# Performance work log

Measured on AMD Instinct MI355X. Metric: run time of the kernel, lower is better.

## Reference

```python
import jax, jax.numpy as jnp
import numpy as np

H = 16   # num_heads
K = 2    # top_k experts per token


def _layer_norm(x, g, b, eps=1e-5):
    mu = jnp.mean(x, axis=-1, keepdims=True)
    var = jnp.mean(jnp.square(x - mu), axis=-1, keepdims=True)
    return (x - mu) * jax.lax.rsqrt(var + eps) * g + b


def setup_inputs() -> dict:
    key = jax.random.key(0)
    ks = jax.random.split(key, 8)
    B, S, D, E = 2, 2048, 1024, 8
    sc = 0.02
    return {
        "x": jax.random.normal(ks[0], (B, S, D), jnp.float32),
        "wq": jax.random.normal(ks[1], (D, D), jnp.float32) * sc,
        "wk": jax.random.normal(ks[2], (D, D), jnp.float32) * sc,
        "wv": jax.random.normal(ks[3], (D, D), jnp.float32) * sc,
        "wo": jax.random.normal(ks[4], (D, D), jnp.float32) * sc,
        "ln1_g": jnp.ones((D,), jnp.float32),
        "ln1_b": jnp.zeros((D,), jnp.float32),
        "ln2_g": jnp.ones((D,), jnp.float32),
        "ln2_b": jnp.zeros((D,), jnp.float32),
        "router_w": jax.random.normal(ks[5], (E, D), jnp.float32) * sc,
        "expert_w": jax.random.normal(ks[6], (E, D, D), jnp.float32) * sc,
    }


def reference(x, wq, wk, wv, wo, ln1_g, ln1_b, ln2_g, ln2_b, router_w, expert_w):
    B, S, D = x.shape
    E = expert_w.shape[0]
    hd = D // H

    # ---- attention sublayer: x = x + attn(norm1(x)) ----
    h = _layer_norm(x, ln1_g, ln1_b)
    q = (h @ wq.T).reshape(B, S, H, hd).transpose(0, 2, 1, 3)  # bhsd
    k = (h @ wk.T).reshape(B, S, H, hd).transpose(0, 2, 1, 3)
    v = (h @ wv.T).reshape(B, S, H, hd).transpose(0, 2, 1, 3)
    scores = jnp.einsum("bhqd,bhkd->bhqk", q, k) / jnp.sqrt(jnp.float32(hd))
    causal = jnp.tril(jnp.ones((S, S), dtype=bool))
    scores = jnp.where(causal, scores, jnp.finfo(scores.dtype).min)
    probs = jax.nn.softmax(scores, axis=-1)
    attn = jnp.einsum("bhqk,bhkd->bhqd", probs, v)
    attn = attn.transpose(0, 2, 1, 3).reshape(B, S, D) @ wo.T
    x = x + attn

    # ---- MoE sublayer: x = x + moe(norm2(x)) ----
    h2 = _layer_norm(x, ln2_g, ln2_b)
    logits = jnp.einsum("bsd,ed->bse", h2, router_w)          # [B,S,E]
    top_logits, top_ids = jax.lax.top_k(logits, K)            # [B,S,K]
    gates = jax.nn.softmax(top_logits, axis=-1)               # [B,S,K]
    # dense combine weights over experts (E is small): sum_k gate_k * onehot(id_k)
    combine = jnp.sum(jax.nn.one_hot(top_ids, E, dtype=h2.dtype) * gates[..., None], axis=-2)  # [B,S,E]
    # per-token matvec with expert weights: token @ W_e.T for each expert, then weighted sum
    y = jnp.einsum("bsd,eod->bseo", h2, expert_w)             # [B,S,E,D]
    moe_out = jnp.einsum("bse,bseo->bso", combine, y)
    return x + moe_out
```

## Files before the change

kernel.cpp:

```cpp
#include <hip/hip_runtime.h>
#include <hip/hip_bf16.h>
#include <cstdint>


typedef __bf16 bf16;
typedef __bf16 bf16x8 __attribute__((ext_vector_type(8)));
typedef float f32x4 __attribute__((ext_vector_type(4)));

#define MFMA(a, b, c) __builtin_amdgcn_mfma_f32_16x16x32_bf16(a, b, c, 0, 0, 0)

__device__ __forceinline__ void gld16(void* lds, const void* g) {
  __builtin_amdgcn_global_load_lds(
      (const __attribute__((address_space(1))) void*)g,
      (__attribute__((address_space(3))) void*)lds, 16, 0, 0);
}

__global__ void split_f32(const float* __restrict__ s, bf16* __restrict__ hi,
                          bf16* __restrict__ lo, int n) {
  int i = (blockIdx.x * 256 + threadIdx.x) * 4;
  if (i >= n) return;
  float4 v = *(const float4*)(s + i);
  float a[4] = {v.x, v.y, v.z, v.w};
#pragma unroll
  for (int j = 0; j < 4; j++) {
    bf16 h = (bf16)a[j];
    hi[i + j] = h;
    lo[i + j] = (bf16)(a[j] - (float)h);
  }
}

__global__ void cvt_f32(const float* __restrict__ s, bf16* __restrict__ hi, int n) {
  int i = (blockIdx.x * 256 + threadIdx.x) * 4;
  if (i >= n) return;
  float4 v = *(const float4*)(s + i);
  hi[i] = (bf16)v.x; hi[i + 1] = (bf16)v.y;
  hi[i + 2] = (bf16)v.z; hi[i + 3] = (bf16)v.w;
}

__global__ void ln_split(const float* __restrict__ x, const float* __restrict__ g,
                         const float* __restrict__ b, bf16* __restrict__ hi,
                         bf16* __restrict__ lo) {
  int tok = blockIdx.x, t = threadIdx.x;
  float4 v = ((const float4*)(x + (size_t)tok * 1024))[t];
  float s = v.x + v.y + v.z + v.w;
  float ss = v.x * v.x + v.y * v.y + v.z * v.z + v.w * v.w;
#pragma unroll
  for (int o = 1; o < 64; o <<= 1) { s += __shfl_xor(s, o); ss += __shfl_xor(ss, o); }
  __shared__ float red[8];
  int w = t >> 6, lane = t & 63;
  if (lane == 0) { red[w] = s; red[4 + w] = ss; }
  __syncthreads();
  s = red[0] + red[1] + red[2] + red[3];
  ss = red[4] + red[5] + red[6] + red[7];
  float mu = s * (1.f / 1024.f);
  float rstd = rsqrtf(ss * (1.f / 1024.f) - mu * mu + 1e-5f);
  float4 gv = ((const float4*)g)[t], bv = ((const float4*)b)[t];
  float y[4] = {(v.x - mu) * rstd * gv.x + bv.x, (v.y - mu) * rstd * gv.y + bv.y,
                (v.z - mu) * rstd * gv.z + bv.z, (v.w - mu) * rstd * gv.w + bv.w};
  size_t o = (size_t)tok * 1024 + t * 4;
#pragma unroll
  for (int j = 0; j < 4; j++) {
    bf16 h = (bf16)y[j];
    hi[o + j] = h;
    lo[o + j] = (bf16)(y[j] - (float)h);
  }
}

__global__ void ln2f(const float* __restrict__ x, const float* __restrict__ g,
                     const float* __restrict__ b, float* __restrict__ h2f,
                     bf16* __restrict__ h2h) {
  int tok = blockIdx.x, t = threadIdx.x;
  float4 v = ((const float4*)(x + (size_t)tok * 1024))[t];
  float s = v.x + v.y + v.z + v.w;
  float ss = v.x * v.x + v.y * v.y + v.z * v.z + v.w * v.w;
#pragma unroll
  for (int o = 1; o < 64; o <<= 1) { s += __shfl_xor(s, o); ss += __shfl_xor(ss, o); }
  __shared__ float red[8];
  int w = t >> 6, lane = t & 63;
  if (lane == 0) { red[w] = s; red[4 + w] = ss; }
  __syncthreads();
  s = red[0] + red[1] + red[2] + red[3];
  ss = red[4] + red[5] + red[6] + red[7];
  float mu = s * (1.f / 1024.f);
  float rstd = rsqrtf(ss * (1.f / 1024.f) - mu * mu + 1e-5f);
  float4 gv = ((const float4*)g)[t], bv = ((const float4*)b)[t];
  float4 y;
  y.x = (v.x - mu) * rstd * gv.x + bv.x;
  y.y = (v.y - mu) * rstd * gv.y + bv.y;
  y.z = (v.z - mu) * rstd * gv.z + bv.z;
  y.w = (v.w - mu) * rstd * gv.w + bv.w;
  ((float4*)(h2f + (size_t)tok * 1024))[t] = y;
  size_t o = (size_t)tok * 1024 + t * 4;
  h2h[o] = (bf16)y.x; h2h[o + 1] = (bf16)y.y;
  h2h[o + 2] = (bf16)y.z; h2h[o + 3] = (bf16)y.w;
}

__global__ void route_wave(const float* __restrict__ h2f,
                           const float* __restrict__ rw, int* __restrict__ eid,
                           float2* __restrict__ gout) {
  int wid = (blockIdx.x * 256 + threadIdx.x) >> 6;
  int lane = threadIdx.x & 63;
  const float4* xr = (const float4*)(h2f + (size_t)wid * 1024);
  float acc[8] = {0.f, 0.f, 0.f, 0.f, 0.f, 0.f, 0.f, 0.f};
#pragma unroll
  for (int it = 0; it < 4; it++) {
    float4 xv = xr[lane + 64 * it];
#pragma unroll
    for (int e = 0; e < 8; e++) {
      float4 wv = ((const float4*)(rw + e * 1024))[lane + 64 * it];
      acc[e] += xv.x * wv.x + xv.y * wv.y + xv.z * wv.z + xv.w * wv.w;
    }
  }
#pragma unroll
  for (int e = 0; e < 8; e++)
#pragma unroll
    for (int o = 1; o < 64; o <<= 1) acc[e] += __shfl_xor(acc[e], o);
  if (lane == 0) {
    int i0 = 0; float l0 = acc[0];
#pragma unroll
    for (int e = 1; e < 8; e++) if (acc[e] > l0) { l0 = acc[e]; i0 = e; }
    int i1 = -1; float l1 = -3e38f;
#pragma unroll
    for (int e = 0; e < 8; e++) if (e != i0 && acc[e] > l1) { l1 = acc[e]; i1 = e; }
    float e1 = __expf(l1 - l0);
    float den = 1.f + e1;
    eid[wid] = i0 | (i1 << 4);
    gout[wid] = make_float2(1.f / den, e1 / den);
  }
}

__global__ void build_lists(const int* __restrict__ eid,
                            const float2* __restrict__ gv,
                            int* __restrict__ tlist, float* __restrict__ glist,
                            int* __restrict__ cnt) {
  int e = blockIdx.x, t = threadIdx.x;
  int lane = t & 63, w = t >> 6;
  __shared__ int wt[4];
  int base = 0;
  for (int c = 0; c < 16; c++) {
    int tok = c * 256 + t;
    int pair = eid[tok];
    int e0 = pair & 15, e1 = pair >> 4;
    bool p = (e0 == e) || (e1 == e);
    float2 g2 = gv[tok];
    float gate = (e0 == e) ? g2.x : g2.y;
    unsigned long long m = __ballot(p);
    int rank = __popcll(m & ((1ull << lane) - 1ull));
    if (lane == 0) wt[w] = __popcll(m);
    __syncthreads();
    int off = base;
    for (int i = 0; i < w; i++) off += wt[i];
    if (p) {
      tlist[e * 4096 + off + rank] = tok;
      glist[e * 4096 + off + rank] = gate;
    }
    base += wt[0] + wt[1] + wt[2] + wt[3];
    __syncthreads();
  }
  if (t == 0) cnt[e] = base;
  int pad = (base + 127) & ~127;
  if (pad > 4096) pad = 4096;
  for (int i = base + t; i < pad; i += 256) {
    tlist[e * 4096 + i] = 0;
    glist[e * 4096 + i] = 0.f;
  }
}

__device__ __forceinline__ void gemm_core_split(
    const bf16* __restrict__ Ah, const bf16* __restrict__ Al,
    const bf16* __restrict__ Bh, const bf16* __restrict__ Bl, int m0, int n0,
    f32x4 (&acc)[4][4]) {
  __shared__ __align__(16) bf16 As_h[4096], As_l[4096], Bs_h[4096], Bs_l[4096];
  int t = threadIdx.x, lane = t & 63, w = t >> 6;
  int i0 = t, i1 = t + 256;
  const bf16* a0h = Ah + (size_t)(m0 + (i0 >> 2)) * 1024 + (i0 & 3) * 8;
  const bf16* a1h = Ah + (size_t)(m0 + (i1 >> 2)) * 1024 + (i1 & 3) * 8;
  const bf16* a0l = Al + (size_t)(m0 + (i0 >> 2)) * 1024 + (i0 & 3) * 8;
  const bf16* a1l = Al + (size_t)(m0 + (i1 >> 2)) * 1024 + (i1 & 3) * 8;
  const bf16* b0h = Bh + (size_t)(n0 + (i0 >> 2)) * 1024 + (i0 & 3) * 8;
  const bf16* b1h = Bh + (size_t)(n0 + (i1 >> 2)) * 1024 + (i1 & 3) * 8;
  const bf16* b0l = Bl + (size_t)(n0 + (i0 >> 2)) * 1024 + (i0 & 3) * 8;
  const bf16* b1l = Bl + (size_t)(n0 + (i1 >> 2)) * 1024 + (i1 & 3) * 8;
  int wm = (w >> 1) * 64, wn = (w & 1) * 64;
  int lr = lane & 15, lq = lane >> 4;
  for (int k0 = 0; k0 < 1024; k0 += 32) {
    __syncthreads();
    gld16(&As_h[i0 * 8], a0h + k0); gld16(&As_h[i1 * 8], a1h + k0);
    gld16(&As_l[i0 * 8], a0l + k0); gld16(&As_l[i1 * 8], a1l + k0);
    gld16(&Bs_h[i0 * 8], b0h + k0); gld16(&Bs_h[i1 * 8], b1h + k0);
    gld16(&Bs_l[i0 * 8], b0l + k0); gld16(&Bs_l[i1 * 8], b1l + k0);
    __syncthreads();
    bf16x8 ah[4], al4[4], bh[4], bl4[4];
#pragma unroll
    for (int i = 0; i < 4; i++) {
      ah[i]  = *(const bf16x8*)&As_h[(wm + i * 16 + lr) * 32 + lq * 8];
      al4[i] = *(const bf16x8*)&As_l[(wm + i * 16 + lr) * 32 + lq * 8];
      bh[i]  = *(const bf16x8*)&Bs_h[(wn + i * 16 + lr) * 32 + lq * 8];
      bl4[i] = *(const bf16x8*)&Bs_l[(wn + i * 16 + lr) * 32 + lq * 8];
    }
#pragma unroll
    for (int i = 0; i < 4; i++)
#pragma unroll
      for (int j = 0; j < 4; j++) {
        f32x4 c = acc[i][j];
        c = MFMA(ah[i], bh[j], c);
        c = MFMA(ah[i], bl4[j], c);
        c = MFMA(al4[i], bh[j], c);
        acc[i][j] = c;
      }
  }
}

__global__ __launch_bounds__(256, 2) void gemm_qkv(
    const bf16* __restrict__ hh, const bf16* __restrict__ hl,
    const bf16* __restrict__ wqh, const bf16* __restrict__ wql,
    const bf16* __restrict__ wkh, const bf16* __restrict__ wkl,
    const bf16* __restrict__ wvh, const bf16* __restrict__ wvl,
    bf16* __restrict__ qh, bf16* __restrict__ ql, bf16* __restrict__ kh,
    bf16* __restrict__ kl, bf16* __restrict__ vh, bf16* __restrict__ vl) {
  int n0 = blockIdx.x * 128, m0 = blockIdx.y * 128, z = blockIdx.z;
  const bf16 *Bh = wqh, *Bl = wql;
  bf16 *Oh = qh, *Ol = ql;
  if (z == 1) { Bh = wkh; Bl = wkl; Oh = kh; Ol = kl; }
  if (z == 2) { Bh = wvh; Bl = wvl; Oh = vh; Ol = vl; }
  float scale = (z == 0) ? (0.125f * 1.44269504f) : 1.0f;
  f32x4 acc[4][4];
#pragma unroll
  for (int i = 0; i < 4; i++)
#pragma unroll
    for (int j = 0; j < 4; j++) acc[i][j] = (f32x4){0.f, 0.f, 0.f, 0.f};
  gemm_core_split(hh, hl, Bh, Bl, m0, n0, acc);
  int t = threadIdx.x, lane = t & 63, w = t >> 6;
  int wm = (w >> 1) * 64, wn = (w & 1) * 64, lr = lane & 15, lq = lane >> 4;
#pragma unroll
  for (int i = 0; i < 4; i++)
#pragma unroll
    for (int j = 0; j < 4; j++)
#pragma unroll
      for (int r = 0; r < 4; r++) {
        size_t row = m0 + wm + i * 16 + lq * 4 + r;
        int col = n0 + wn + j * 16 + lr;
        float v = acc[i][j][r] * scale;
        bf16 h = (bf16)v;
        Oh[row * 1024 + col] = h;
        Ol[row * 1024 + col] = (bf16)(v - (float)h);
      }
}

__global__ __launch_bounds__(256, 2) void gemm_wo(
    const bf16* __restrict__ ah, const bf16* __restrict__ al,
    const bf16* __restrict__ bh, const bf16* __restrict__ bl,
    const float* __restrict__ resid, float* __restrict__ outp) {
  int n0 = blockIdx.x * 128, m0 = blockIdx.y * 128;
  f32x4 acc[4][4];
#pragma unroll
  for (int i = 0; i < 4; i++)
#pragma unroll
    for (int j = 0; j < 4; j++) acc[i][j] = (f32x4){0.f, 0.f, 0.f, 0.f};
  gemm_core_split(ah, al, bh, bl, m0, n0, acc);
  int t = threadIdx.x, lane = t & 63, w = t >> 6;
  int wm = (w >> 1) * 64, wn = (w & 1) * 64, lr = lane & 15, lq = lane >> 4;
#pragma unroll
  for (int i = 0; i < 4; i++)
#pragma unroll
    for (int j = 0; j < 4; j++)
#pragma unroll
      for (int r = 0; r < 4; r++) {
        size_t row = m0 + wm + i * 16 + lq * 4 + r;
        int col = n0 + wn + j * 16 + lr;
        outp[row * 1024 + col] = resid[row * 1024 + col] + acc[i][j][r];
      }
}

__global__ void vtrans(const bf16* __restrict__ vh, const bf16* __restrict__ vl,
                       bf16* __restrict__ vth, bf16* __restrict__ vtl) {
  int bh = blockIdx.y, s0 = blockIdx.x * 64;
  int b = bh >> 4, h = bh & 15;
  int t = threadIdx.x;
  __shared__ __align__(16) bf16 tile[4096];
  int r = t >> 2, c4 = t & 3;
  int dr = t >> 2, tg = t & 3;
#pragma unroll
  for (int pass = 0; pass < 2; pass++) {
    const bf16* src = pass ? vl : vh;
    bf16* dst = pass ? vtl : vth;
    if (pass) __syncthreads();
    const bf16* sp = src + (size_t)(b * 2048 + s0 + r) * 1024 + h * 64 + c4 * 16;
    bf16x8 v0 = *(const bf16x8*)sp;
    bf16x8 v1 = *(const bf16x8*)(sp + 8);
#pragma unroll
    for (int j = 0; j < 8; j++) {
      int d0 = c4 * 16 + j, d1 = c4 * 16 + 8 + j;
      tile[d0 * 64 + (r ^ ((d0 >> 3) << 3))] = v0[j];
      tile[d1 * 64 + (r ^ ((d1 >> 3) << 3))] = v1[j];
    }
    __syncthreads();
#pragma unroll
    for (int hf = 0; hf < 2; hf++) {
      int tok = tg * 16 + hf * 8;
      bf16x8 o = *(const bf16x8*)&tile[dr * 64 + (tok ^ ((dr >> 3) << 3))];
      *(bf16x8*)(dst + (size_t)(bh * 64 + dr) * 2048 + s0 + tok) = o;
    }
  }
}

__global__ __launch_bounds__(256, 2) void attn_fused(
    const bf16* __restrict__ qh, const bf16* __restrict__ ql,
    const bf16* __restrict__ kh, const bf16* __restrict__ kl,
    const bf16* __restrict__ vth, const bf16* __restrict__ vtl,
    bf16* __restrict__ oh, bf16* __restrict__ ol) {
  const int S = 2048, D = 1024;
  int qt = 15 - blockIdx.y;
  int hb = blockIdx.x;
  int head = hb & 15, b = hb >> 4;
  int qb = qt * 128;
  int t = threadIdx.x, lane = t & 63, w = t >> 6;
  int lr = lane & 15, lq = lane >> 4;
  int base = b * S, hcol = head * 64;

  __shared__ __align__(16) bf16 Kh_s[4096], Kl_s[4096];
  __shared__ __align__(16) bf16 Vh_s[4096], Vl_s[4096];
  __shared__ __align__(16) bf16 Ph_s[4][1024], Pl_s[4][1024];

  bf16x8 qfh[2][2], qfl[2][2];
#pragma unroll
  for (int qr = 0; qr < 2; qr++) {
    const bf16* p1 = qh + (size_t)(base + qb + w * 32 + qr * 16 + lr) * D + hcol + lq * 8;
    const bf16* p2 = ql + (size_t)(base + qb + w * 32 + qr * 16 + lr) * D + hcol + lq * 8;
    qfh[qr][0] = *(const bf16x8*)p1; qfh[qr][1] = *(const bf16x8*)(p1 + 32);
    qfl[qr][0] = *(const bf16x8*)p2; qfl[qr][1] = *(const bf16x8*)(p2 + 32);
  }
  f32x4 O[2][4];
  float lrow[2][4];
#pragma unroll
  for (int qr = 0; qr < 2; qr++)
#pragma unroll
    for (int j = 0; j < 4; j++) {
      O[qr][j] = (f32x4){0.f, 0.f, 0.f, 0.f};
      lrow[qr][j] = 0.f;
    }

  int r0 = t >> 3, p0 = t & 7;
  int r1 = (t + 256) >> 3, p1 = (t + 256) & 7;
  int g0 = p0 ^ (r0 & 7), g1 = p1 ^ (r1 & 7);
  const bf16* k0hp = kh + (size_t)(base + r0) * D + hcol + g0 * 8;
  const bf16* k1hp = kh + (size_t)(base + r1) * D + hcol + g1 * 8;
  const bf16* k0lp = kl + (size_t)(base + r0) * D + hcol + g0 * 8;
  const bf16* k1lp = kl + (size_t)(base + r1) * D + hcol + g1 * 8;
  const bf16* v0hp = vth + (size_t)(hb * 64 + r0) * 2048 + g0 * 8;
  const bf16* v1hp = vth + (size_t)(hb * 64 + r1) * 2048 + g1 * 8;
  const bf16* v0lp = vtl + (size_t)(hb * 64 + r0) * 2048 + g0 * 8;
  const bf16* v1lp = vtl + (size_t)(hb * 64 + r1) * 2048 + g1 * 8;

  int qwmin = qb + w * 32;
  int pswz = ((lr >> 2) & 1) << 4;

  for (int kt = 0; kt <= qb + 64; kt += 64) {
    __syncthreads();
    gld16(&Kh_s[t * 8], k0hp + (size_t)kt * D);
    gld16(&Kh_s[2048 + t * 8], k1hp + (size_t)kt * D);
    gld16(&Kl_s[t * 8], k0lp + (size_t)kt * D);
    gld16(&Kl_s[2048 + t * 8], k1lp + (size_t)kt * D);
    gld16(&Vh_s[t * 8], v0hp + kt);
    gld16(&Vh_s[2048 + t * 8], v1hp + kt);
    gld16(&Vl_s[t * 8], v0lp + kt);
    gld16(&Vl_s[2048 + t * 8], v1lp + kt);
    __syncthreads();
    if (kt > qwmin + 31) continue;
    bool need_mask = (kt + 63 > qwmin);
#pragma unroll
    for (int hf = 0; hf < 2; hf++) {
      f32x4 sc[2][2];
#pragma unroll
      for (int tt = 0; tt < 2; tt++) {
        int key16 = (hf * 2 + tt) * 16 + lr;
        int gl = (lq ^ (key16 & 7)) * 8;
        int gh = ((4 + lq) ^ (key16 & 7)) * 8;
        bf16x8 k0 = *(const bf16x8*)&Kh_s[key16 * 64 + gl];
        bf16x8 k1 = *(const bf16x8*)&Kh_s[key16 * 64 + gh];
        bf16x8 m0 = *(const bf16x8*)&Kl_s[key16 * 64 + gl];
        bf16x8 m1 = *(const bf16x8*)&Kl_s[key16 * 64 + gh];
#pragma unroll
        for (int qr = 0; qr < 2; qr++) {
          f32x4 s = (f32x4){0.f, 0.f, 0.f, 0.f};
          s = MFMA(qfh[qr][0], k0, s); s = MFMA(qfh[qr][1], k1, s);
          s = MFMA(qfh[qr][0], m0, s); s = MFMA(qfh[qr][1], m1, s);
          s = MFMA(qfl[qr][0], k0, s); s = MFMA(qfl[qr][1], k1, s);
          sc[qr][tt] = s;
        }
      }
#pragma unroll
      for (int qr = 0; qr < 2; qr++)
#pragma unroll
        for (int tt = 0; tt < 2; tt++) {
          int key = kt + (hf * 2 + tt) * 16 + lr;
#pragma unroll
          for (int r = 0; r < 4; r++) {
            float s = sc[qr][tt][r];
            if (need_mask) {
              int q = qwmin + qr * 16 + lq * 4 + r;
              s = (key <= q) ? s : -30000.f;
            }
            float pv = __builtin_amdgcn_exp2f(s);
            lrow[qr][r] += pv;
            bf16 ph = (bf16)pv;
            int col = (tt * 16 + lr) ^ ((lq & 1) << 4);
            int idx = (qr * 16 + lq * 4 + r) * 32 + col;
            Ph_s[w][idx] = ph;
            Pl_s[w][idx] = (bf16)(pv - (float)ph);
          }
        }
      bf16x8 vbh[4], vbl[4];
#pragma unroll
      for (int j = 0; j < 4; j++) {
        int d = j * 16 + lr;
        int gv = ((hf * 4 + lq) ^ (d & 7)) * 8;
        vbh[j] = *(const bf16x8*)&Vh_s[d * 64 + gv];
        vbl[j] = *(const bf16x8*)&Vl_s[d * 64 + gv];
      }
#pragma unroll
      for (int qr = 0; qr < 2; qr++) {
        int poff = (qr * 16 + lr) * 32 + ((lq * 8) ^ pswz);
        bf16x8 pf = *(const bf16x8*)&Ph_s[w][poff];
        bf16x8 pl2 = *(const bf16x8*)&Pl_s[w][poff];
#pragma unroll
        for (int j = 0; j < 4; j++) {
          f32x4 c = O[qr][j];
          c = MFMA(pf, vbh[j], c);
          c = MFMA(pf, vbl[j], c);
          c = MFMA(pl2, vbh[j], c);
          O[qr][j] = c;
        }
      }
    }
  }
#pragma unroll
  for (int qr = 0; qr < 2; qr++) {
    float linv[4];
#pragma unroll
    for (int r = 0; r < 4; r++) {
      float l = lrow[qr][r];
      l += __shfl_xor(l, 1); l += __shfl_xor(l, 2);
      l += __shfl_xor(l, 4); l += __shfl_xor(l, 8);
      linv[r] = 1.f / l;
    }
#pragma unroll
    for (int j = 0; j < 4; j++)
#pragma unroll
      for (int r = 0; r < 4; r++) {
        size_t tok = (size_t)(base + qb + w * 32 + qr * 16 + lq * 4 + r);
        int col = hcol + j * 16 + lr;
        float v = O[qr][j][r] * linv[r];
        bf16 h = (bf16)v;
        oh[tok * D + col] = h;
        ol[tok * D + col] = (bf16)(v - (float)h);
      }
  }
}

__global__ __launch_bounds__(256, 2) void gemm_moe(
    const bf16* __restrict__ A, const bf16* __restrict__ W,
    const int* __restrict__ tlist, const float* __restrict__ glist,
    const int* __restrict__ cnt, float* __restrict__ outp) {
  int e = blockIdx.z;
  int count = cnt[e];
  int m0 = blockIdx.y * 128;
  if (m0 >= count) return;
  int n0 = blockIdx.x * 128;
  const int* tl = tlist + e * 4096;
  const bf16* B = W + (size_t)e * 1024 * 1024;
  __shared__ __align__(16) bf16 As[4096], Bs[4096];
  int t = threadIdx.x, lane = t & 63, w = t >> 6;
  int i0 = t, i1 = t + 256;
  int ra = tl[m0 + (i0 >> 2)], rb = tl[m0 + (i1 >> 2)];
  const bf16* a0 = A + (size_t)ra * 1024 + (i0 & 3) * 8;
  const bf16* a1 = A + (size_t)rb * 1024 + (i1 & 3) * 8;
  const bf16* b0 = B + (size_t)(n0 + (i0 >> 2)) * 1024 + (i0 & 3) * 8;
  const bf16* b1 = B + (size_t)(n0 + (i1 >> 2)) * 1024 + (i1 & 3) * 8;
  int wm = (w >> 1) * 64, wn = (w & 1) * 64, lr = lane & 15, lq = lane >> 4;
  f32x4 acc[4][4];
#pragma unroll
  for (int i = 0; i < 4; i++)
#pragma unroll
    for (int j = 0; j < 4; j++) acc[i][j] = (f32x4){0.f, 0.f, 0.f, 0.f};
  for (int k0 = 0; k0 < 1024; k0 += 32) {
    __syncthreads();
    gld16(&As[i0 * 8], a0 + k0); gld16(&As[i1 * 8], a1 + k0);
    gld16(&Bs[i0 * 8], b0 + k0); gld16(&Bs[i1 * 8], b1 + k0);
    __syncthreads();
    bf16x8 af[4], bfr[4];
#pragma unroll
    for (int i = 0; i < 4; i++) {
      af[i] = *(const bf16x8*)&As[(wm + i * 16 + lr) * 32 + lq * 8];
      bfr[i] = *(const bf16x8*)&Bs[(wn + i * 16 + lr) * 32 + lq * 8];
    }
#pragma unroll
    for (int i = 0; i < 4; i++)
#pragma unroll
      for (int j = 0; j < 4; j++) acc[i][j] = MFMA(af[i], bfr[j], acc[i][j]);
  }
#pragma unroll
  for (int i = 0; i < 4; i++)
#pragma unroll
    for (int r = 0; r < 4; r++) {
      int slot = m0 + wm + i * 16 + lq * 4 + r;
      if (slot < count) {
        int tok = tl[slot];
        float gte = glist[e * 4096 + slot];
#pragma unroll
        for (int j = 0; j < 4; j++) {
          int col = n0 + wn + j * 16 + lr;
          atomicAdd(&outp[(size_t)tok * 1024 + col], gte * acc[i][j][r]);
        }
      }
    }
}

extern "C" void kernel_launch(void* const* d_in, const int* in_sizes, int n_in,
                              void* d_out, int out_size, void* d_ws, size_t ws_size,
                              hipStream_t stream) {
  (void)in_sizes; (void)n_in; (void)out_size; (void)ws_size;
  const float* x    = (const float*)d_in[0];
  const float* wq   = (const float*)d_in[1];
  const float* wk   = (const float*)d_in[2];
  const float* wv   = (const float*)d_in[3];
  const float* wo   = (const float*)d_in[4];
  const float* ln1g = (const float*)d_in[5];
  const float* ln1b = (const float*)d_in[6];
  const float* ln2g = (const float*)d_in[7];
  const float* ln2b = (const float*)d_in[8];
  const float* rw   = (const float*)d_in[9];
  const float* expw = (const float*)d_in[10];
  float* out = (float*)d_out;

  char* p = (char*)d_ws;
  auto take = [&](size_t bytes) -> char* {
    char* r = p;
    p += (bytes + 255) & ~(size_t)255;
    return r;
  };
  const size_t ND2 = 4096ull * 1024 * 2;
  const size_t WD2 = 1024ull * 1024 * 2;
  bf16* h_hi = (bf16*)take(ND2); bf16* h_lo = (bf16*)take(ND2);
  bf16* wqh = (bf16*)take(WD2); bf16* wql = (bf16*)take(WD2);
  bf16* wkh = (bf16*)take(WD2); bf16* wkl = (bf16*)take(WD2);
  bf16* wvh = (bf16*)take(WD2); bf16* wvl = (bf16*)take(WD2);
  bf16* woh = (bf16*)take(WD2); bf16* wol = (bf16*)take(WD2);
  bf16* q_hi = (bf16*)take(ND2); bf16* q_lo = (bf16*)take(ND2);
  bf16* k_hi = (bf16*)take(ND2); bf16* k_lo = (bf16*)take(ND2);
  bf16* v_hi = (bf16*)take(ND2); bf16* v_lo = (bf16*)take(ND2);
  bf16* a_hi = (bf16*)take(ND2); bf16* a_lo = (bf16*)take(ND2);
  bf16* h2h  = (bf16*)take(ND2);
  bf16* ewh  = (bf16*)take(8ull * 1024 * 1024 * 2);
  int*   tlist  = (int*)take(8ull * 4096 * 4);
  float* glist  = (float*)take(8ull * 4096 * 4);
  int*   cnt    = (int*)take(64);
  int*   reid   = (int*)take(4096 * 4);
  float2* rg    = (float2*)take(4096 * 8);
  bf16* vt_hi = h_hi;
  bf16* vt_lo = h_lo;
  float* h2f = (float*)h_hi;

  split_f32<<<1024, 256, 0, stream>>>(wq, wqh, wql, 1048576);
  split_f32<<<1024, 256, 0, stream>>>(wk, wkh, wkl, 1048576);
  split_f32<<<1024, 256, 0, stream>>>(wv, wvh, wvl, 1048576);
  split_f32<<<1024, 256, 0, stream>>>(wo, woh, wol, 1048576);
  cvt_f32<<<8192, 256, 0, stream>>>(expw, ewh, 8388608);

  ln_split<<<4096, 256, 0, stream>>>(x, ln1g, ln1b, h_hi, h_lo);
  gemm_qkv<<<dim3(8, 32, 3), 256, 0, stream>>>(h_hi, h_lo, wqh, wql, wkh, wkl,
                                               wvh, wvl, q_hi, q_lo, k_hi, k_lo,
                                               v_hi, v_lo);
  vtrans<<<dim3(32, 32), 256, 0, stream>>>(v_hi, v_lo, vt_hi, vt_lo);
  attn_fused<<<dim3(32, 16), 256, 0, stream>>>(q_hi, q_lo, k_hi, k_lo, vt_hi,
                                               vt_lo, a_hi, a_lo);
  gemm_wo<<<dim3(8, 32), 256, 0, stream>>>(a_hi, a_lo, woh, wol, x, out);

  ln2f<<<4096, 256, 0, stream>>>(out, ln2g, ln2b, h2f, h2h);
  route_wave<<<1024, 256, 0, stream>>>(h2f, rw, reid, rg);
  build_lists<<<8, 256, 0, stream>>>(reid, rg, tlist, glist, cnt);
  gemm_moe<<<dim3(8, 32, 8), 256, 0, stream>>>(h2h, ewh, tlist, glist, cnt,
                                               out);
}
```

Before: 442.2 us.

## Fuse prep/router kernels, write V transposed from QKV GEMM, use 32x32 MFMA attention

Merges the five weight-conversion launches into one kernel and fuses LayerNorm2 with the router so the fp32 h2 buffer no longer round-trips through global memory. The QKV GEMM now writes V directly in transposed head layout, which removes the separate vtrans kernel. Attention is rebuilt around 32x32x16 MFMA tiles, packing hi/lo P values into one LDS word and skipping the fully masked second key subtile. Together these cut launch count and memory traffic, but the router now computes per token inside a block and the new attention changes register and LDS pressure.

```diff
diff --git a/kernel.cpp b/kernel.cpp
--- a/kernel.cpp
+++ b/kernel.cpp
@@ -5,9 +5,12 @@
 
 typedef __bf16 bf16;
 typedef __bf16 bf16x8 __attribute__((ext_vector_type(8)));
+typedef __bf16 bf16x4 __attribute__((ext_vector_type(4)));
 typedef float f32x4 __attribute__((ext_vector_type(4)));
+typedef float f32x16 __attribute__((ext_vector_type(16)));
 
 #define MFMA(a, b, c) __builtin_amdgcn_mfma_f32_16x16x32_bf16(a, b, c, 0, 0, 0)
+#define MFMA32(a, b, c) __builtin_amdgcn_mfma_f32_32x32x16_bf16(a, b, c, 0, 0, 0)
 
 __device__ __forceinline__ void gld16(void* lds, const void* g) {
   __builtin_amdgcn_global_load_lds(
@@ -15,26 +18,43 @@
       (__attribute__((address_space(3))) void*)lds, 16, 0, 0);
 }
 
-__global__ void split_f32(const float* __restrict__ s, bf16* __restrict__ hi,
-                          bf16* __restrict__ lo, int n) {
-  int i = (blockIdx.x * 256 + threadIdx.x) * 4;
-  if (i >= n) return;
-  float4 v = *(const float4*)(s + i);
-  float a[4] = {v.x, v.y, v.z, v.w};
-#pragma unroll
-  for (int j = 0; j < 4; j++) {
-    bf16 h = (bf16)a[j];
-    hi[i + j] = h;
-    lo[i + j] = (bf16)(a[j] - (float)h);
-  }
-}
-
-__global__ void cvt_f32(const float* __restrict__ s, bf16* __restrict__ hi, int n) {
-  int i = (blockIdx.x * 256 + threadIdx.x) * 4;
-  if (i >= n) return;
-  float4 v = *(const float4*)(s + i);
-  hi[i] = (bf16)v.x; hi[i + 1] = (bf16)v.y;
-  hi[i + 2] = (bf16)v.z; hi[i + 3] = (bf16)v.w;
+__device__ __forceinline__ uint32_t pack_hilo(float pv) {
+  bf16 h = (bf16)pv;
+  bf16 l = (bf16)(pv - (float)h);
+  union { bf16 b[2]; uint32_t u; } cv;
+  cv.b[0] = h; cv.b[1] = l;
+  return cv.u;
+}
+
+__global__ void prep_weights(const float* __restrict__ wq, const float* __restrict__ wk,
+                             const float* __restrict__ wv, const float* __restrict__ wo,
+                             const float* __restrict__ expw,
+                             bf16* __restrict__ wqh, bf16* __restrict__ wql,
+                             bf16* __restrict__ wkh, bf16* __restrict__ wkl,
+                             bf16* __restrict__ wvh, bf16* __restrict__ wvl,
+                             bf16* __restrict__ woh, bf16* __restrict__ wol,
+                             bf16* __restrict__ ewh) {
+  int bid = blockIdx.x;
+  if (bid < 4096) {
+    int wsel = bid >> 10;
+    const float* src = wsel == 0 ? wq : wsel == 1 ? wk : wsel == 2 ? wv : wo;
+    bf16* hi = wsel == 0 ? wqh : wsel == 1 ? wkh : wsel == 2 ? wvh : woh;
+    bf16* lo = wsel == 0 ? wql : wsel == 1 ? wkl : wsel == 2 ? wvl : wol;
+    int i = ((bid & 1023) * 256 + threadIdx.x) * 4;
+    float4 v = *(const float4*)(src + i);
+    float a[4] = {v.x, v.y, v.z, v.w};
+#pragma unroll
+    for (int j = 0; j < 4; j++) {
+      bf16 h = (bf16)a[j];
+      hi[i + j] = h;
+      lo[i + j] = (bf16)(a[j] - (float)h);
+    }
+  } else {
+    int i = ((bid - 4096) * 256 + threadIdx.x) * 4;
+    float4 v = *(const float4*)(expw + i);
+    ewh[i] = (bf16)v.x; ewh[i + 1] = (bf16)v.y;
+    ewh[i + 2] = (bf16)v.z; ewh[i + 3] = (bf16)v.w;
+  }
 }
 
 __global__ void ln_split(const float* __restrict__ x, const float* __restrict__ g,
@@ -66,16 +86,19 @@
   }
 }
 
-__global__ void ln2f(const float* __restrict__ x, const float* __restrict__ g,
-                     const float* __restrict__ b, float* __restrict__ h2f,
-                     bf16* __restrict__ h2h) {
+__global__ void ln2route(const float* __restrict__ x1, const float* __restrict__ g,
+                         const float* __restrict__ b, const float* __restrict__ rw,
+                         bf16* __restrict__ h2h, int* __restrict__ eid,
+                         float2* __restrict__ gout) {
   int tok = blockIdx.x, t = threadIdx.x;
-  float4 v = ((const float4*)(x + (size_t)tok * 1024))[t];
+  float4 v = ((const float4*)(x1 + (size_t)tok * 1024))[t];
   float s = v.x + v.y + v.z + v.w;
   float ss = v.x * v.x + v.y * v.y + v.z * v.z + v.w * v.w;
 #pragma unroll
   for (int o = 1; o < 64; o <<= 1) { s += __shfl_xor(s, o); ss += __shfl_xor(ss, o); }
   __shared__ float red[8];
+  __shared__ float h2s[1024];
+  __shared__ float lg[8];
   int w = t >> 6, lane = t & 63;
   if (lane == 0) { red[w] = s; red[4 + w] = ss; }
   __syncthreads();
@@ -89,43 +112,40 @@
   y.y = (v.y - mu) * rstd * gv.y + bv.y;
   y.z = (v.z - mu) * rstd * gv.z + bv.z;
   y.w = (v.w - mu) * rstd * gv.w + bv.w;
-  ((float4*)(h2f + (size_t)tok * 1024))[t] = y;
+  ((float4*)h2s)[t] = y;
   size_t o = (size_t)tok * 1024 + t * 4;
   h2h[o] = (bf16)y.x; h2h[o + 1] = (bf16)y.y;
   h2h[o + 2] = (bf16)y.z; h2h[o + 3] = (bf16)y.w;
-}
-
-__global__ void route_wave(const float* __restrict__ h2f,
-                           const float* __restrict__ rw, int* __restrict__ eid,
-                           float2* __restrict__ gout) {
-  int wid = (blockIdx.x * 256 + threadIdx.x) >> 6;
-  int lane = threadIdx.x & 63;
-  const float4* xr = (const float4*)(h2f + (size_t)wid * 1024);
-  float acc[8] = {0.f, 0.f, 0.f, 0.f, 0.f, 0.f, 0.f, 0.f};
+  __syncthreads();
+  float a0 = 0.f, a1 = 0.f;
+  const float4* r0 = (const float4*)(rw + (2 * w) * 1024);
+  const float4* r1 = (const float4*)(rw + (2 * w + 1) * 1024);
 #pragma unroll
   for (int it = 0; it < 4; it++) {
-    float4 xv = xr[lane + 64 * it];
-#pragma unroll
-    for (int e = 0; e < 8; e++) {
-      float4 wv = ((const float4*)(rw + e * 1024))[lane + 64 * it];
-      acc[e] += xv.x * wv.x + xv.y * wv.y + xv.z * wv.z + xv.w * wv.w;
-    }
-  }
-#pragma unroll
-  for (int e = 0; e < 8; e++)
-#pragma unroll
-    for (int o = 1; o < 64; o <<= 1) acc[e] += __shfl_xor(acc[e], o);
-  if (lane == 0) {
-    int i0 = 0; float l0 = acc[0];
-#pragma unroll
-    for (int e = 1; e < 8; e++) if (acc[e] > l0) { l0 = acc[e]; i0 = e; }
+    float4 xv = ((const float4*)h2s)[lane + 64 * it];
+    float4 w0 = r0[lane + 64 * it];
+    float4 w1 = r1[lane + 64 * it];
+    a0 += xv.x * w0.x + xv.y * w0.y + xv.z * w0.z + xv.w * w0.w;
+    a1 += xv.x * w1.x + xv.y * w1.y + xv.z * w1.z + xv.w * w1.w;
+  }
+#pragma unroll
+  for (int o2 = 1; o2 < 64; o2 <<= 1) {
+    a0 += __shfl_xor(a0, o2);
+    a1 += __shfl_xor(a1, o2);
+  }
+  if (lane == 0) { lg[2 * w] = a0; lg[2 * w + 1] = a1; }
+  __syncthreads();
+  if (t == 0) {
+    int i0 = 0; float l0 = lg[0];
+#pragma unroll
+    for (int e = 1; e < 8; e++) if (lg[e] > l0) { l0 = lg[e]; i0 = e; }
     int i1 = -1; float l1 = -3e38f;
 #pragma unroll
-    for (int e = 0; e < 8; e++) if (e != i0 && acc[e] > l1) { l1 = acc[e]; i1 = e; }
+    for (int e = 0; e < 8; e++) if (e != i0 && lg[e] > l1) { l1 = lg[e]; i1 = e; }
     float e1 = __expf(l1 - l0);
     float den = 1.f + e1;
-    eid[wid] = i0 | (i1 << 4);
-    gout[wid] = make_float2(1.f / den, e1 / den);
+    eid[tok] = i0 | (i1 << 4);
+    gout[tok] = make_float2(1.f / den, e1 / den);
   }
 }
 
@@ -217,13 +237,11 @@
     const bf16* __restrict__ wkh, const bf16* __restrict__ wkl,
     const bf16* __restrict__ wvh, const bf16* __restrict__ wvl,
     bf16* __restrict__ qh, bf16* __restrict__ ql, bf16* __restrict__ kh,
-    bf16* __restrict__ kl, bf16* __restrict__ vh, bf16* __restrict__ vl) {
+    bf16* __restrict__ kl, bf16* __restrict__ vth, bf16* __restrict__ vtl) {
   int n0 = blockIdx.x * 128, m0 = blockIdx.y * 128, z = blockIdx.z;
   const bf16 *Bh = wqh, *Bl = wql;
-  bf16 *Oh = qh, *Ol = ql;
-  if (z == 1) { Bh = wkh; Bl = wkl; Oh = kh; Ol = kl; }
-  if (z == 2) { Bh = wvh; Bl = wvl; Oh = vh; Ol = vl; }
-  float scale = (z == 0) ? (0.125f * 1.44269504f) : 1.0f;
+  if (z == 1) { Bh = wkh; Bl = wkl; }
+  if (z == 2) { Bh = wvh; Bl = wvl; }
   f32x4 acc[4][4];
 #pragma unroll
   for (int i = 0; i < 4; i++)
@@ -232,19 +250,46 @@
   gemm_core_split(hh, hl, Bh, Bl, m0, n0, acc);
   int t = threadIdx.x, lane = t & 63, w = t >> 6;
   int wm = (w >> 1) * 64, wn = (w & 1) * 64, lr = lane & 15, lq = lane >> 4;
-#pragma unroll
-  for (int i = 0; i < 4; i++)
-#pragma unroll
-    for (int j = 0; j < 4; j++)
-#pragma unroll
-      for (int r = 0; r < 4; r++) {
-        size_t row = m0 + wm + i * 16 + lq * 4 + r;
+  if (z < 2) {
+    bf16* Oh = z == 0 ? qh : kh;
+    bf16* Ol = z == 0 ? ql : kl;
+    float scale = (z == 0) ? (0.125f * 1.44269504f) : 1.0f;
+#pragma unroll
+    for (int i = 0; i < 4; i++)
+#pragma unroll
+      for (int j = 0; j < 4; j++)
+#pragma unroll
+        for (int r = 0; r < 4; r++) {
+          size_t row = m0 + wm + i * 16 + lq * 4 + r;
+          int col = n0 + wn + j * 16 + lr;
+          float v = acc[i][j][r] * scale;
+          bf16 h = (bf16)v;
+          Oh[row * 1024 + col] = h;
+          Ol[row * 1024 + col] = (bf16)(v - (float)h);
+        }
+  } else {
+    int bb = m0 >> 11;
+    int srow0 = m0 & 2047;
+#pragma unroll
+    for (int i = 0; i < 4; i++)
+#pragma unroll
+      for (int j = 0; j < 4; j++) {
         int col = n0 + wn + j * 16 + lr;
-        float v = acc[i][j][r] * scale;
-        bf16 h = (bf16)v;
-        Oh[row * 1024 + col] = h;
-        Ol[row * 1024 + col] = (bf16)(v - (float)h);
-      }
+        int head = col >> 6, d = col & 63;
+        int s = srow0 + wm + i * 16 + lq * 4;
+        bf16x4 hv, lv;
+#pragma unroll
+        for (int r = 0; r < 4; r++) {
+          float v = acc[i][j][r];
+          bf16 h = (bf16)v;
+          hv[r] = h;
+          lv[r] = (bf16)(v - (float)h);
+        }
+        size_t off = ((size_t)((bb * 16 + head) * 64 + d)) * 2048 + s;
+        *(bf16x4*)(vth + off) = hv;
+        *(bf16x4*)(vtl + off) = lv;
+      }
+  }
 }
 
 __global__ __launch_bounds__(256, 2) void gemm_wo(
@@ -270,38 +315,6 @@
         int col = n0 + wn + j * 16 + lr;
         outp[row * 1024 + col] = resid[row * 1024 + col] + acc[i][j][r];
       }
-}
-
-__global__ void vtrans(const bf16* __restrict__ vh, const bf16* __restrict__ vl,
-                       bf16* __restrict__ vth, bf16* __restrict__ vtl) {
-  int bh = blockIdx.y, s0 = blockIdx.x * 64;
-  int b = bh >> 4, h = bh & 15;
-  int t = threadIdx.x;
-  __shared__ __align__(16) bf16 tile[4096];
-  int r = t >> 2, c4 = t & 3;
-  int dr = t >> 2, tg = t & 3;
-#pragma unroll
-  for (int pass = 0; pass < 2; pass++) {
-    const bf16* src = pass ? vl : vh;
-    bf16* dst = pass ? vtl : vth;
-    if (pass) __syncthreads();
-    const bf16* sp = src + (size_t)(b * 2048 + s0 + r) * 1024 + h * 64 + c4 * 16;
-    bf16x8 v0 = *(const bf16x8*)sp;
-    bf16x8 v1 = *(const bf16x8*)(sp + 8);
-#pragma unroll
-    for (int j = 0; j < 8; j++) {
-      int d0 = c4 * 16 + j, d1 = c4 * 16 + 8 + j;
-      tile[d0 * 64 + (r ^ ((d0 >> 3) << 3))] = v0[j];
-      tile[d1 * 64 + (r ^ ((d1 >> 3) << 3))] = v1[j];
-    }
-    __syncthreads();
-#pragma unroll
-    for (int hf = 0; hf < 2; hf++) {
-      int tok = tg * 16 + hf * 8;
-      bf16x8 o = *(const bf16x8*)&tile[dr * 64 + (tok ^ ((dr >> 3) << 3))];
-      *(bf16x8*)(dst + (size_t)(bh * 64 + dr) * 2048 + s0 + tok) = o;
-    }
-  }
 }
 
 __global__ __launch_bounds__(256, 2) void attn_fused(
@@ -315,45 +328,41 @@
   int head = hb & 15, b = hb >> 4;
   int qb = qt * 128;
   int t = threadIdx.x, lane = t & 63, w = t >> 6;
-  int lr = lane & 15, lq = lane >> 4;
+  int l31 = lane & 31, l5 = lane >> 5;
   int base = b * S, hcol = head * 64;
 
   __shared__ __align__(16) bf16 Kh_s[4096], Kl_s[4096];
   __shared__ __align__(16) bf16 Vh_s[4096], Vl_s[4096];
-  __shared__ __align__(16) bf16 Ph_s[4][1024], Pl_s[4][1024];
-
-  bf16x8 qfh[2][2], qfl[2][2];
-#pragma unroll
-  for (int qr = 0; qr < 2; qr++) {
-    const bf16* p1 = qh + (size_t)(base + qb + w * 32 + qr * 16 + lr) * D + hcol + lq * 8;
-    const bf16* p2 = ql + (size_t)(base + qb + w * 32 + qr * 16 + lr) * D + hcol + lq * 8;
-    qfh[qr][0] = *(const bf16x8*)p1; qfh[qr][1] = *(const bf16x8*)(p1 + 32);
-    qfl[qr][0] = *(const bf16x8*)p2; qfl[qr][1] = *(const bf16x8*)(p2 + 32);
-  }
-  f32x4 O[2][4];
-  float lrow[2][4];
-#pragma unroll
-  for (int qr = 0; qr < 2; qr++)
-#pragma unroll
-    for (int j = 0; j < 4; j++) {
-      O[qr][j] = (f32x4){0.f, 0.f, 0.f, 0.f};
-      lrow[qr][j] = 0.f;
-    }
+  __shared__ __align__(16) uint32_t Pp[4][32 * 68];
+
+  bf16x8 qfh[4], qfl[4];
+  {
+    const bf16* p1 = qh + (size_t)(base + qb + w * 32 + l31) * D + hcol + l5 * 8;
+    const bf16* p2 = ql + (size_t)(base + qb + w * 32 + l31) * D + hcol + l5 * 8;
+#pragma unroll
+    for (int c = 0; c < 4; c++) {
+      qfh[c] = *(const bf16x8*)(p1 + 16 * c);
+      qfl[c] = *(const bf16x8*)(p2 + 16 * c);
+    }
+  }
+  f32x16 O0, O1;
+  float lrow[16];
+#pragma unroll
+  for (int r = 0; r < 16; r++) { O0[r] = 0.f; O1[r] = 0.f; lrow[r] = 0.f; }
 
   int r0 = t >> 3, p0 = t & 7;
-  int r1 = (t + 256) >> 3, p1 = (t + 256) & 7;
-  int g0 = p0 ^ (r0 & 7), g1 = p1 ^ (r1 & 7);
+  int r1 = 32 + r0;
+  int g0 = p0 ^ (r0 & 7);
   const bf16* k0hp = kh + (size_t)(base + r0) * D + hcol + g0 * 8;
-  const bf16* k1hp = kh + (size_t)(base + r1) * D + hcol + g1 * 8;
+  const bf16* k1hp = kh + (size_t)(base + r1) * D + hcol + g0 * 8;
   const bf16* k0lp = kl + (size_t)(base + r0) * D + hcol + g0 * 8;
-  const bf16* k1lp = kl + (size_t)(base + r1) * D + hcol + g1 * 8;
+  const bf16* k1lp = kl + (size_t)(base + r1) * D + hcol + g0 * 8;
   const bf16* v0hp = vth + (size_t)(hb * 64 + r0) * 2048 + g0 * 8;
-  const bf16* v1hp = vth + (size_t)(hb * 64 + r1) * 2048 + g1 * 8;
+  const bf16* v1hp = vth + (size_t)(hb * 64 + r1) * 2048 + g0 * 8;
   const bf16* v0lp = vtl + (size_t)(hb * 64 + r0) * 2048 + g0 * 8;
-  const bf16* v1lp = vtl + (size_t)(hb * 64 + r1) * 2048 + g1 * 8;
+  const bf16* v1lp = vtl + (size_t)(hb * 64 + r1) * 2048 + g0 * 8;
 
   int qwmin = qb + w * 32;
-  int pswz = ((lr >> 2) & 1) << 4;
 
   for (int kt = 0; kt <= qb + 64; kt += 64) {
     __syncthreads();
@@ -367,94 +376,84 @@
     gld16(&Vl_s[2048 + t * 8], v1lp + kt);
     __syncthreads();
     if (kt > qwmin + 31) continue;
-    bool need_mask = (kt + 63 > qwmin);
-#pragma unroll
-    for (int hf = 0; hf < 2; hf++) {
-      f32x4 sc[2][2];
-#pragma unroll
-      for (int tt = 0; tt < 2; tt++) {
-        int key16 = (hf * 2 + tt) * 16 + lr;
-        int gl = (lq ^ (key16 & 7)) * 8;
-        int gh = ((4 + lq) ^ (key16 & 7)) * 8;
-        bf16x8 k0 = *(const bf16x8*)&Kh_s[key16 * 64 + gl];
-        bf16x8 k1 = *(const bf16x8*)&Kh_s[key16 * 64 + gh];
-        bf16x8 m0 = *(const bf16x8*)&Kl_s[key16 * 64 + gl];
-        bf16x8 m1 = *(const bf16x8*)&Kl_s[key16 * 64 + gh];
-#pragma unroll
-        for (int qr = 0; qr < 2; qr++) {
-          f32x4 s = (f32x4){0.f, 0.f, 0.f, 0.f};
-          s = MFMA(qfh[qr][0], k0, s); s = MFMA(qfh[qr][1], k1, s);
-          s = MFMA(qfh[qr][0], m0, s); s = MFMA(qfh[qr][1], m1, s);
-          s = MFMA(qfl[qr][0], k0, s); s = MFMA(qfl[qr][1], k1, s);
-          sc[qr][tt] = s;
+    bool mask0 = (kt + 31 > qwmin);
+    bool skip1 = (kt + 32 > qwmin + 31);
+    bool mask1 = (kt + 63 > qwmin);
+#pragma unroll
+    for (int ktile = 0; ktile < 2; ktile++) {
+      if (ktile == 1 && skip1) break;
+      int keyr = ktile * 32 + l31;
+      f32x16 sc;
+#pragma unroll
+      for (int r = 0; r < 16; r++) sc[r] = 0.f;
+#pragma unroll
+      for (int c = 0; c < 4; c++) {
+        int dg = ((2 * c + l5) ^ (keyr & 7)) * 8;
+        bf16x8 kv = *(const bf16x8*)&Kh_s[keyr * 64 + dg];
+        bf16x8 km = *(const bf16x8*)&Kl_s[keyr * 64 + dg];
+        sc = MFMA32(qfh[c], kv, sc);
+        sc = MFMA32(qfl[c], kv, sc);
+        sc = MFMA32(qfh[c], km, sc);
+      }
+      bool m = ktile ? mask1 : mask0;
+      int keyg = kt + keyr;
+      uint32_t* prow = &Pp[w][ktile * 32 + l31];
+#pragma unroll
+      for (int r = 0; r < 16; r++) {
+        int qlocal = (r & 3) + 8 * (r >> 2) + 4 * l5;
+        float sv = sc[r];
+        if (m && keyg > qwmin + qlocal) sv = -30000.f;
+        float pv = __builtin_amdgcn_exp2f(sv);
+        lrow[r] += pv;
+        prow[qlocal * 68] = pack_hilo(pv);
+      }
+    }
+#pragma unroll
+    for (int c = 0; c < 4; c++) {
+      if (skip1 && c >= 2) break;
+      const uint32_t* pr = &Pp[w][l31 * 68 + 16 * c + l5 * 8];
+      uint32_t pd[8];
+      *(uint4*)&pd[0] = *(const uint4*)&pr[0];
+      *(uint4*)&pd[4] = *(const uint4*)&pr[4];
+      union { uint32_t u[4]; bf16x8 v; } ph_, pl_;
+#pragma unroll
+      for (int i = 0; i < 4; i++) {
+        ph_.u[i] = __builtin_amdgcn_perm(pd[2 * i + 1], pd[2 * i], 0x05040100u);
+        pl_.u[i] = __builtin_amdgcn_perm(pd[2 * i + 1], pd[2 * i], 0x07060302u);
+      }
+#pragma unroll
+      for (int dtile = 0; dtile < 2; dtile++) {
+        int d = dtile * 32 + l31;
+        int kg = ((2 * c + l5) ^ (d & 7)) * 8;
+        bf16x8 vb = *(const bf16x8*)&Vh_s[d * 64 + kg];
+        bf16x8 vm = *(const bf16x8*)&Vl_s[d * 64 + kg];
+        if (dtile == 0) {
+          O0 = MFMA32(ph_.v, vb, O0);
+          O0 = MFMA32(pl_.v, vb, O0);
+          O0 = MFMA32(ph_.v, vm, O0);
+        } else {
+          O1 = MFMA32(ph_.v, vb, O1);
+          O1 = MFMA32(pl_.v, vb, O1);
+          O1 = MFMA32(ph_.v, vm, O1);
         }
       }
-#pragma unroll
-      for (int qr = 0; qr < 2; qr++)
-#pragma unroll
-        for (int tt = 0; tt < 2; tt++) {
-          int key = kt + (hf * 2 + tt) * 16 + lr;
-#pragma unroll
-          for (int r = 0; r < 4; r++) {
-            float s = sc[qr][tt][r];
-            if (need_mask) {
-              int q = qwmin + qr * 16 + lq * 4 + r;
-              s = (key <= q) ? s : -30000.f;
-            }
-            float pv = __builtin_amdgcn_exp2f(s);
-            lrow[qr][r] += pv;
-            bf16 ph = (bf16)pv;
-            int col = (tt * 16 + lr) ^ ((lq & 1) << 4);
-            int idx = (qr * 16 + lq * 4 + r) * 32 + col;
-            Ph_s[w][idx] = ph;
-            Pl_s[w][idx] = (bf16)(pv - (float)ph);
-          }
-        }
-      bf16x8 vbh[4], vbl[4];
-#pragma unroll
-      for (int j = 0; j < 4; j++) {
-        int d = j * 16 + lr;
-        int gv = ((hf * 4 + lq) ^ (d & 7)) * 8;
-        vbh[j] = *(const bf16x8*)&Vh_s[d * 64 + gv];
-        vbl[j] = *(const bf16x8*)&Vl_s[d * 64 + gv];
-      }
-#pragma unroll
-      for (int qr = 0; qr < 2; qr++) {
-        int poff = (qr * 16 + lr) * 32 + ((lq * 8) ^ pswz);
-        bf16x8 pf = *(const bf16x8*)&Ph_s[w][poff];
-        bf16x8 pl2 = *(const bf16x8*)&Pl_s[w][poff];
-#pragma unroll
-        for (int j = 0; j < 4; j++) {
-          f32x4 c = O[qr][j];
-          c = MFMA(pf, vbh[j], c);
-          c = MFMA(pf, vbl[j], c);
-          c = MFMA(pl2, vbh[j], c);
-          O[qr][j] = c;
-        }
-      }
-    }
-  }
-#pragma unroll
-  for (int qr = 0; qr < 2; qr++) {
-    float linv[4];
-#pragma unroll
-    for (int r = 0; r < 4; r++) {
-      float l = lrow[qr][r];
-      l += __shfl_xor(l, 1); l += __shfl_xor(l, 2);
-      l += __shfl_xor(l, 4); l += __shfl_xor(l, 8);
-      linv[r] = 1.f / l;
-    }
-#pragma unroll
-    for (int j = 0; j < 4; j++)
-#pragma unroll
-      for (int r = 0; r < 4; r++) {
-        size_t tok = (size_t)(base + qb + w * 32 + qr * 16 + lq * 4 + r);
-        int col = hcol + j * 16 + lr;
-        float v = O[qr][j][r] * linv[r];
-        bf16 h = (bf16)v;
-        oh[tok * D + col] = h;
-        ol[tok * D + col] = (bf16)(v - (float)h);
-      }
+    }
+  }
+#pragma unroll
+  for (int r = 0; r < 16; r++) {
+    float l = lrow[r];
+    l += __shfl_xor(l, 1); l += __shfl_xor(l, 2); l += __shfl_xor(l, 4);
+    l += __shfl_xor(l, 8); l += __shfl_xor(l, 16);
+    float linv = 1.f / l;
+    int qlocal = (r & 3) + 8 * (r >> 2) + 4 * l5;
+    size_t tok = (size_t)(base + qb + w * 32 + qlocal);
+    float v0 = O0[r] * linv;
+    float v1 = O1[r] * linv;
+    bf16 h0 = (bf16)v0, h1 = (bf16)v1;
+    oh[tok * D + hcol + l31] = h0;
+    ol[tok * D + hcol + l31] = (bf16)(v0 - (float)h0);
+    oh[tok * D + hcol + 32 + l31] = h1;
+    ol[tok * D + hcol + 32 + l31] = (bf16)(v1 - (float)h1);
   }
 }
 
@@ -548,7 +547,7 @@
   bf16* woh = (bf16*)take(WD2); bf16* wol = (bf16*)take(WD2);
   bf16* q_hi = (bf16*)take(ND2); bf16* q_lo = (bf16*)take(ND2);
   bf16* k_hi = (bf16*)take(ND2); bf16* k_lo = (bf16*)take(ND2);
-  bf16* v_hi = (bf16*)take(ND2); bf16* v_lo = (bf16*)take(ND2);
+  bf16* vt_hi = (bf16*)take(ND2); bf16* vt_lo = (bf16*)take(ND2);
   bf16* a_hi = (bf16*)take(ND2); bf16* a_lo = (bf16*)take(ND2);
   bf16* h2h  = (bf16*)take(ND2);
   bf16* ewh  = (bf16*)take(8ull * 1024 * 1024 * 2);
@@ -557,27 +556,17 @@
   int*   cnt    = (int*)take(64);
   int*   reid   = (int*)take(4096 * 4);
   float2* rg    = (float2*)take(4096 * 8);
-  bf16* vt_hi = h_hi;
-  bf16* vt_lo = h_lo;
-  float* h2f = (float*)h_hi;
-
-  split_f32<<<1024, 256, 0, stream>>>(wq, wqh, wql, 1048576);
-  split_f32<<<1024, 256, 0, stream>>>(wk, wkh, wkl, 1048576);
-  split_f32<<<1024, 256, 0, stream>>>(wv, wvh, wvl, 1048576);
-  split_f32<<<1024, 256, 0, stream>>>(wo, woh, wol, 1048576);
-  cvt_f32<<<8192, 256, 0, stream>>>(expw, ewh, 8388608);
-
+
+  prep_weights<<<12288, 256, 0, stream>>>(wq, wk, wv, wo, expw, wqh, wql, wkh,
+                                          wkl, wvh, wvl, woh, wol, ewh);
   ln_split<<<4096, 256, 0, stream>>>(x, ln1g, ln1b, h_hi, h_lo);
   gemm_qkv<<<dim3(8, 32, 3), 256, 0, stream>>>(h_hi, h_lo, wqh, wql, wkh, wkl,
                                                wvh, wvl, q_hi, q_lo, k_hi, k_lo,
-                                               v_hi, v_lo);
-  vtrans<<<dim3(32, 32), 256, 0, stream>>>(v_hi, v_lo, vt_hi, vt_lo);
+                                               vt_hi, vt_lo);
   attn_fused<<<dim3(32, 16), 256, 0, stream>>>(q_hi, q_lo, k_hi, k_lo, vt_hi,
                                                vt_lo, a_hi, a_lo);
   gemm_wo<<<dim3(8, 32), 256, 0, stream>>>(a_hi, a_lo, woh, wol, x, out);
-
-  ln2f<<<4096, 256, 0, stream>>>(out, ln2g, ln2b, h2f, h2h);
-  route_wave<<<1024, 256, 0, stream>>>(h2f, rw, reid, rg);
+  ln2route<<<4096, 256, 0, stream>>>(out, ln2g, ln2b, rw, h2h, reid, rg);
   build_lists<<<8, 256, 0, stream>>>(reid, rg, tlist, glist, cnt);
   gemm_moe<<<dim3(8, 32, 8), 256, 0, stream>>>(h2h, ewh, tlist, glist, cnt,
                                                out);
```

Measured after the change: 414.6 us. 6.2% less time.
